# Kernel tuning notes

Hardware: AMD Instinct MI355X
Metric: run time of the kernel (lower is better)

## Reference

```python
import jax, jax.numpy as jnp
import numpy as np

D_MODEL, Q, V, H = 1024, 64, 64, 16
B, K = 2, 2048


def setup_inputs() -> dict:
    key = jax.random.key(0)
    ks = jax.random.split(key, 8)
    s = 0.02
    return {
        "xi": jax.random.normal(ks[0], (B, K, D_MODEL), dtype=jnp.float32),
        # stacked per-head projection weights (equivalent to h separate nn.Linear)
        "Wq": jax.random.normal(ks[1], (H, D_MODEL, Q), dtype=jnp.float32) * s,
        "bq": jax.random.normal(ks[2], (H, Q), dtype=jnp.float32) * s,
        "Wk": jax.random.normal(ks[3], (H, D_MODEL, Q), dtype=jnp.float32) * s,
        "bk": jax.random.normal(ks[4], (H, Q), dtype=jnp.float32) * s,
        "Wv": jax.random.normal(ks[5], (H, D_MODEL, V), dtype=jnp.float32) * s,
        "bv": jax.random.normal(ks[6], (H, V), dtype=jnp.float32) * s,
        "Wo": jax.random.normal(ks[7], (H * V, D_MODEL), dtype=jnp.float32) * s,
        "bo": jnp.zeros((D_MODEL,), dtype=jnp.float32),
    }


def reference(xi, Wq, bq, Wk, bk, Wv, bv, Wo, bo):
    # per-head projections, batched over heads: [B,H,K,q]
    queries = jnp.einsum("bkd,hdq->bhkq", xi, Wq) + bq[None, :, None, :]
    keys = jnp.einsum("bkd,hdq->bhkq", xi, Wk) + bk[None, :, None, :]
    values = jnp.einsum("bkd,hdv->bhkv", xi, Wv) + bv[None, :, None, :]
    # NOTE: original scales by sqrt(queries.shape[1]) == sqrt(seq_len K), not sqrt(q)
    scale = 1.0 / np.sqrt(xi.shape[1]).astype(np.float32)
    scores = jax.nn.softmax(jnp.einsum("bhkq,bhmq->bhkm", queries, keys) * scale, axis=-1)
    attn = jnp.einsum("bhkm,bhmv->bhkv", scores, values)  # [B,H,K,v]
    # concat heads along last dim -> [B,K,H*v]
    attn = attn.transpose(0, 2, 1, 3).reshape(xi.shape[0], xi.shape[1], -1)
    return attn @ Wo + bo
```

## Files before the change

kernel.cpp:

```cpp
#include <hip/hip_runtime.h>
#include <math.h>

typedef __bf16 bf16x8 __attribute__((ext_vector_type(8)));
typedef float  f32x4  __attribute__((ext_vector_type(4)));
typedef float  f32x16 __attribute__((ext_vector_type(16)));
typedef unsigned short u16x8 __attribute__((ext_vector_type(8)));

#define D_MODEL 1024
#define QDIM    64
#define HEADS   16
#define BATCH   2
#define SEQ     2048
#define M_ROWS  (BATCH*SEQ)
#define NCAT    (HEADS*3*QDIM)

__device__ __forceinline__ unsigned short f2bf(float f) {
    unsigned int u = __float_as_uint(f);
    u += 0x7fffu + ((u >> 16) & 1u);
    return (unsigned short)(u >> 16);
}

__device__ __forceinline__ void gl16(const unsigned short* g, unsigned short* l) {
    __builtin_amdgcn_global_load_lds(
        (const __attribute__((address_space(1))) unsigned int*)g,
        (__attribute__((address_space(3))) unsigned int*)l, 16, 0, 0);
}

__global__ __launch_bounds__(256) void k_cvt_bf16(const float* __restrict__ in,
                                                  unsigned short* __restrict__ out) {
    int i = (blockIdx.x * 256 + threadIdx.x) * 8;
    f32x4 a = *(const f32x4*)(in + i);
    f32x4 b = *(const f32x4*)(in + i + 4);
    u16x8 o;
    o[0]=f2bf(a[0]); o[1]=f2bf(a[1]); o[2]=f2bf(a[2]); o[3]=f2bf(a[3]);
    o[4]=f2bf(b[0]); o[5]=f2bf(b[1]); o[6]=f2bf(b[2]); o[7]=f2bf(b[3]);
    *(u16x8*)(out + i) = o;
}

__global__ __launch_bounds__(256) void k_prep_wcat(const float* __restrict__ Wq,
                                                   const float* __restrict__ Wk,
                                                   const float* __restrict__ Wv,
                                                   const float* __restrict__ bq,
                                                   const float* __restrict__ bk,
                                                   const float* __restrict__ bv,
                                                   unsigned short* __restrict__ WcatT,
                                                   float* __restrict__ bcat,
                                                   float qscale) {
    int blk = blockIdx.x;
    int dt = blk & 15, h = (blk >> 4) & 15, s = blk >> 8;
    const float* W = (s == 0) ? Wq : (s == 1) ? Wk : Wv;
    float sc = (s == 0) ? qscale : 1.0f;
    __shared__ float t[64][65];
    int tid = threadIdx.x;
    int dr = tid >> 2, qc = (tid & 3) * 16;
    const float* src = W + (size_t)h * (D_MODEL * QDIM) + (size_t)(dt * 64 + dr) * QDIM + qc;
#pragma unroll
    for (int j = 0; j < 4; ++j) {
        f32x4 v = *(const f32x4*)(src + j * 4);
        t[dr][qc + j * 4 + 0] = v[0]; t[dr][qc + j * 4 + 1] = v[1];
        t[dr][qc + j * 4 + 2] = v[2]; t[dr][qc + j * 4 + 3] = v[3];
    }
    __syncthreads();
    int q = tid >> 2, dc = (tid & 3) * 16;
    unsigned short* dst = WcatT + (size_t)(h * 192 + s * 64 + q) * D_MODEL + dt * 64 + dc;
#pragma unroll
    for (int j = 0; j < 2; ++j) {
        u16x8 o;
#pragma unroll
        for (int e = 0; e < 8; ++e) o[e] = f2bf(t[dc + j * 8 + e][q] * sc);
        *(u16x8*)(dst + j * 8) = o;
    }
    if (dt == 0 && tid < 64) {
        const float* bb = (s == 0) ? bq : (s == 1) ? bk : bv;
        bcat[h * 192 + s * 64 + tid] = bb[h * QDIM + tid] * sc;
    }
}

__global__ __launch_bounds__(256) void k_prep_wo(const float* __restrict__ Wo,
                                                 unsigned short* __restrict__ WoT) {
    int blk = blockIdx.x;
    int ct = blk & 15, rt = blk >> 4;
    __shared__ float t[64][65];
    int tid = threadIdx.x;
    int dr = tid >> 2, qc = (tid & 3) * 16;
    const float* src = Wo + (size_t)(rt * 64 + dr) * D_MODEL + ct * 64 + qc;
#pragma unroll
    for (int j = 0; j < 4; ++j) {
        f32x4 v = *(const f32x4*)(src + j * 4);
        t[dr][qc + j * 4 + 0] = v[0]; t[dr][qc + j * 4 + 1] = v[1];
        t[dr][qc + j * 4 + 2] = v[2]; t[dr][qc + j * 4 + 3] = v[3];
    }
    __syncthreads();
    int q = tid >> 2, dc = (tid & 3) * 16;
    unsigned short* dst = WoT + (size_t)(ct * 64 + q) * D_MODEL + rt * 64 + dc;
#pragma unroll
    for (int j = 0; j < 2; ++j) {
        u16x8 o;
#pragma unroll
        for (int e = 0; e < 8; ++e) o[e] = f2bf(t[dc + j * 8 + e][q]);
        *(u16x8*)(dst + j * 8) = o;
    }
}

template<bool OUT_BF16>
__global__ __launch_bounds__(256) void k_gemm(const unsigned short* __restrict__ A,
                                              const unsigned short* __restrict__ BT,
                                              const float* __restrict__ bias,
                                              void* __restrict__ Cout,
                                              int N, int Kd) {
    __shared__ __align__(16) unsigned short Alds[128 * 64];
    __shared__ __align__(16) unsigned short Blds[128 * 64];
    const int tid = threadIdx.x;
    const int lane = tid & 63, w = tid >> 6;
    const int g = lane >> 4, c = lane & 15;
    int nwg = gridDim.x * gridDim.y;
    int bid = blockIdx.y * gridDim.x + blockIdx.x;
    int sw = (bid & 7) * (nwg >> 3) + (bid >> 3);
    int bx = sw % gridDim.x, by = sw / gridDim.x;
    const int m0 = by * 128, n0 = bx * 128;
    const int wm = (w >> 1) * 64, wn = (w & 1) * 64;
    const int r8 = lane >> 3, chx = (lane & 7) ^ r8;
    const int swz = c & 7;
    f32x4 acc[4][4] = {};

    for (int k0 = 0; k0 < Kd; k0 += 64) {
        __builtin_amdgcn_sched_barrier(0);
        __builtin_amdgcn_s_barrier();
#pragma unroll
        for (int i = 0; i < 4; ++i) {
            int row = w * 32 + i * 8 + r8;
            gl16(A + (size_t)(m0 + row) * Kd + k0 + chx * 8, Alds + w * 2048 + i * 512);
            gl16(BT + (size_t)(n0 + row) * Kd + k0 + chx * 8, Blds + w * 2048 + i * 512);
        }
        asm volatile("s_waitcnt vmcnt(0)" ::: "memory");
        __builtin_amdgcn_s_barrier();
        __builtin_amdgcn_sched_barrier(0);
#pragma unroll
        for (int kk = 0; kk < 2; ++kk) {
            bf16x8 af[4], bfr[4];
#pragma unroll
            for (int mf = 0; mf < 4; ++mf) {
                int row = wm + mf * 16 + c;
                af[mf] = *(const bf16x8*)(Alds + row * 64 + (((kk * 4 + g) ^ swz) * 8));
            }
#pragma unroll
            for (int nf = 0; nf < 4; ++nf) {
                int row = wn + nf * 16 + c;
                bfr[nf] = *(const bf16x8*)(Blds + row * 64 + (((kk * 4 + g) ^ swz) * 8));
            }
            __builtin_amdgcn_s_setprio(1);
#pragma unroll
            for (int mf = 0; mf < 4; ++mf)
#pragma unroll
                for (int nf = 0; nf < 4; ++nf)
                    acc[mf][nf] = __builtin_amdgcn_mfma_f32_16x16x32_bf16(af[mf], bfr[nf], acc[mf][nf], 0, 0, 0);
            __builtin_amdgcn_s_setprio(0);
        }
    }

#pragma unroll
    for (int mf = 0; mf < 4; ++mf)
#pragma unroll
        for (int nf = 0; nf < 4; ++nf) {
            int col = n0 + wn + nf * 16 + c;
            float bb = bias[col];
#pragma unroll
            for (int r = 0; r < 4; ++r) {
                int row = m0 + wm + mf * 16 + 4 * g + r;
                float v = acc[mf][nf][r] + bb;
                if (OUT_BF16)
                    ((unsigned short*)Cout)[(size_t)row * N + col] = f2bf(v);
                else
                    ((float*)Cout)[(size_t)row * N + col] = v;
            }
        }
}

__global__ __launch_bounds__(256) void k_repack(const unsigned short* __restrict__ qkv,
                                                unsigned short* __restrict__ kfrag,
                                                unsigned short* __restrict__ vfrag) {
    int blk = blockIdx.x;
    int kt = blk & 31, h = (blk >> 5) & 15, b = blk >> 9;
    __shared__ unsigned short ktile[64][72];
    __shared__ unsigned short vtile[64][72];
    int tid = threadIdx.x;
#pragma unroll
    for (int j = 0; j < 2; ++j) {
        int cid = tid + j * 256;
        int row = cid >> 3, ch = (cid & 7) * 8;
        const unsigned short* base = qkv + (size_t)(b * SEQ + kt * 64 + row) * NCAT + h * 192;
        *(u16x8*)&ktile[row][ch] = *(const u16x8*)(base + 64 + ch);
        *(u16x8*)&vtile[row][ch] = *(const u16x8*)(base + 128 + ch);
    }
    __syncthreads();
    size_t obase = (size_t)blk * 4096;
#pragma unroll
    for (int j = 0; j < 2; ++j) {
        int p = tid + j * 256;
        int f = p >> 6, l31 = p & 31, hi = (p >> 5) & 1;
        *(u16x8*)(kfrag + obase + p * 8) =
            *(const u16x8*)&ktile[(f >> 2) * 32 + l31][(f & 3) * 16 + hi * 8];
        int vv = (f & 1) * 32 + l31;
        int k0 = (f >> 2) * 32 + ((f >> 1) & 1) * 16 + hi * 8;
        u16x8 o;
#pragma unroll
        for (int e = 0; e < 8; ++e) o[e] = vtile[k0 + e][vv];
        *(u16x8*)(vfrag + obase + p * 8) = o;
    }
}

__global__ __launch_bounds__(256) void k_attn(const unsigned short* __restrict__ qkv,
                                              const unsigned short* __restrict__ kfrag,
                                              const unsigned short* __restrict__ vfrag,
                                              unsigned short* __restrict__ attn) {
    int bid = blockIdx.x;
    int blk = (bid & 7) * 128 + (bid >> 3);
    int qt = blk & 31, h = (blk >> 5) & 15, b = blk >> 9;
    int tid = threadIdx.x, w = tid >> 6, lane = tid & 63;
    int l31 = lane & 31, hi = lane >> 5;
    int qh = w & 1, kh = w >> 1;

    __shared__ __align__(16) unsigned char KV[2][16384];

    const int qbase = b * SEQ + qt * 64;
    const unsigned short* qrow = qkv + (size_t)(qbase + qh * 32 + l31) * NCAT + h * 192;
    bf16x8 qf[4];
#pragma unroll
    for (int s = 0; s < 4; ++s) qf[s] = *(const bf16x8*)(qrow + s * 16 + hi * 8);

    f32x16 o0 = {}, o1 = {};
    float rsum = 0.f;

    const size_t fb = (size_t)(b * 512 + h * 32) * 4096;
    const unsigned short* ks0 = kfrag + fb + (w)     * 512 + lane * 8;
    const unsigned short* ks1 = kfrag + fb + (w + 4) * 512 + lane * 8;
    const unsigned short* vs0 = vfrag + fb + (w)     * 512 + lane * 8;
    const unsigned short* vs1 = vfrag + fb + (w + 4) * 512 + lane * 8;
    const unsigned kd0 = w * 1024, kd1 = (w + 4) * 1024;
    const unsigned vd0 = 8192 + w * 1024, vd1 = 8192 + (w + 4) * 1024;
    const int lx = lane * 16;

    gl16(ks0, (unsigned short*)&KV[0][kd0]);
    gl16(vs0, (unsigned short*)&KV[0][vd0]);
    gl16(ks1, (unsigned short*)&KV[0][kd1]);
    gl16(vs1, (unsigned short*)&KV[0][vd1]);
    ks0 += 4096; ks1 += 4096; vs0 += 4096; vs1 += 4096;
    asm volatile("s_waitcnt vmcnt(0)" ::: "memory");
    __builtin_amdgcn_s_barrier();

    const int NT = SEQ / 64;
    for (int t = 0; t < NT; ++t) {
        const int cur = t & 1;
        if (t + 1 < NT) {
            gl16(ks0, (unsigned short*)&KV[cur ^ 1][kd0]);
            gl16(vs0, (unsigned short*)&KV[cur ^ 1][vd0]);
            gl16(ks1, (unsigned short*)&KV[cur ^ 1][kd1]);
            gl16(vs1, (unsigned short*)&KV[cur ^ 1][vd1]);
            ks0 += 4096; ks1 += 4096; vs0 += 4096; vs1 += 4096;
            asm volatile("s_waitcnt vmcnt(4)" ::: "memory");
        } else {
            asm volatile("s_waitcnt vmcnt(0)" ::: "memory");
        }
        __builtin_amdgcn_s_barrier();
        __builtin_amdgcn_sched_barrier(0);

        const unsigned char* Kf = &KV[cur][0];
        const unsigned char* Vf = &KV[cur][8192];

        f32x16 st = {};
        __builtin_amdgcn_s_setprio(1);
#pragma unroll
        for (int s = 0; s < 4; ++s) {
            bf16x8 kf = *(const bf16x8*)(Kf + (kh * 4 + s) * 1024 + lx);
            st = __builtin_amdgcn_mfma_f32_32x32x16_bf16(kf, qf[s], st, 0, 0, 0);
        }
        __builtin_amdgcn_s_setprio(0);

#pragma unroll
        for (int r = 0; r < 16; ++r) {
            float p = __builtin_amdgcn_exp2f(st[r]);
            st[r] = p;
            rsum += p;
        }
        unsigned int d0, d1, d2, d3, d4, d5, d6, d7;
        asm("v_cvt_pk_bf16_f32 %0, %1, %2" : "=v"(d0) : "v"(st[0]),  "v"(st[1]));
        asm("v_cvt_pk_bf16_f32 %0, %1, %2" : "=v"(d1) : "v"(st[2]),  "v"(st[3]));
        asm("v_cvt_pk_bf16_f32 %0, %1, %2" : "=v"(d2) : "v"(st[4]),  "v"(st[5]));
        asm("v_cvt_pk_bf16_f32 %0, %1, %2" : "=v"(d3) : "v"(st[6]),  "v"(st[7]));
        asm("v_cvt_pk_bf16_f32 %0, %1, %2" : "=v"(d4) : "v"(st[8]),  "v"(st[9]));
        asm("v_cvt_pk_bf16_f32 %0, %1, %2" : "=v"(d5) : "v"(st[10]), "v"(st[11]));
        asm("v_cvt_pk_bf16_f32 %0, %1, %2" : "=v"(d6) : "v"(st[12]), "v"(st[13]));
        asm("v_cvt_pk_bf16_f32 %0, %1, %2" : "=v"(d7) : "v"(st[14]), "v"(st[15]));
        asm("v_permlane32_swap_b32 %0, %1" : "+v"(d0), "+v"(d2));
        asm("v_permlane32_swap_b32 %0, %1" : "+v"(d1), "+v"(d3));
        asm("v_permlane32_swap_b32 %0, %1" : "+v"(d4), "+v"(d6));
        asm("v_permlane32_swap_b32 %0, %1" : "+v"(d5), "+v"(d7));
        union { unsigned int u[4]; bf16x8 v; } pa0, pa1;
        pa0.u[0] = d0; pa0.u[1] = d1; pa0.u[2] = d2; pa0.u[3] = d3;
        pa1.u[0] = d4; pa1.u[1] = d5; pa1.u[2] = d6; pa1.u[3] = d7;

        __builtin_amdgcn_s_setprio(1);
        {
            bf16x8 vf00 = *(const bf16x8*)(Vf + (kh * 4 + 0) * 1024 + lx);
            bf16x8 vf01 = *(const bf16x8*)(Vf + (kh * 4 + 1) * 1024 + lx);
            bf16x8 vf10 = *(const bf16x8*)(Vf + (kh * 4 + 2) * 1024 + lx);
            bf16x8 vf11 = *(const bf16x8*)(Vf + (kh * 4 + 3) * 1024 + lx);
            o0 = __builtin_amdgcn_mfma_f32_32x32x16_bf16(pa0.v, vf00, o0, 0, 0, 0);
            o1 = __builtin_amdgcn_mfma_f32_32x32x16_bf16(pa0.v, vf01, o1, 0, 0, 0);
            o0 = __builtin_amdgcn_mfma_f32_32x32x16_bf16(pa1.v, vf10, o0, 0, 0, 0);
            o1 = __builtin_amdgcn_mfma_f32_32x32x16_bf16(pa1.v, vf11, o1, 0, 0, 0);
        }
        __builtin_amdgcn_s_setprio(0);
        __builtin_amdgcn_sched_barrier(0);
        __builtin_amdgcn_s_barrier();
    }

    rsum += __shfl_xor(rsum, 32);
    __syncthreads();
    float* red = (float*)&KV[0][0];
    float* rsb = (float*)&KV[1][0];
    if (kh == 1) {
#pragma unroll
        for (int r = 0; r < 16; ++r) {
            int q = (r & 3) + 8 * (r >> 2) + 4 * hi;
            red[(qh * 32 + q) * 64 + l31]      = o0[r];
            red[(qh * 32 + q) * 64 + 32 + l31] = o1[r];
        }
    }
    if (lane < 32) rsb[(kh * 2 + qh) * 32 + l31] = rsum;
    __syncthreads();
    if (kh == 0) {
#pragma unroll
        for (int r = 0; r < 16; ++r) {
            int q = (r & 3) + 8 * (r >> 2) + 4 * hi;
            float tot = rsb[qh * 32 + q] + rsb[(2 + qh) * 32 + q];
            float inv = 1.0f / tot;
            float v0 = (o0[r] + red[(qh * 32 + q) * 64 + l31]) * inv;
            float v1 = (o1[r] + red[(qh * 32 + q) * 64 + 32 + l31]) * inv;
            int row = qbase + qh * 32 + q;
            attn[(size_t)row * (HEADS * QDIM) + h * QDIM + l31]      = f2bf(v0);
            attn[(size_t)row * (HEADS * QDIM) + h * QDIM + 32 + l31] = f2bf(v1);
        }
    }
}

extern "C" void kernel_launch(void* const* d_in, const int* in_sizes, int n_in,
                              void* d_out, int out_size, void* d_ws, size_t ws_size,
                              hipStream_t stream) {
    const float* xi = (const float*)d_in[0];
    const float* Wq = (const float*)d_in[1];
    const float* bq = (const float*)d_in[2];
    const float* Wk = (const float*)d_in[3];
    const float* bk = (const float*)d_in[4];
    const float* Wv = (const float*)d_in[5];
    const float* bv = (const float*)d_in[6];
    const float* Wo = (const float*)d_in[7];
    const float* bo = (const float*)d_in[8];

    unsigned short* xi_bf = (unsigned short*)d_ws;
    unsigned short* WcatT = xi_bf + (size_t)M_ROWS * D_MODEL;
    unsigned short* WoT   = WcatT + (size_t)NCAT * D_MODEL;
    float*          bcat  = (float*)(WoT + (size_t)D_MODEL * D_MODEL);
    unsigned short* qkvc  = (unsigned short*)(bcat + NCAT);
    unsigned short* kfrag = qkvc + (size_t)M_ROWS * NCAT;
    unsigned short* vfrag = kfrag + (size_t)BATCH * HEADS * 32 * 4096;
    unsigned short* attnb = vfrag + (size_t)BATCH * HEADS * 32 * 4096;

    float qscale = 1.4426950408889634f / sqrtf((float)SEQ);

    k_cvt_bf16<<<(M_ROWS * D_MODEL) / 2048, 256, 0, stream>>>(xi, xi_bf);
    k_prep_wcat<<<768, 256, 0, stream>>>(Wq, Wk, Wv, bq, bk, bv, WcatT, bcat, qscale);
    k_prep_wo<<<256, 256, 0, stream>>>(Wo, WoT);

    k_gemm<true><<<dim3(NCAT / 128, M_ROWS / 128), 256, 0, stream>>>(
        xi_bf, WcatT, bcat, (void*)qkvc, NCAT, D_MODEL);

    k_repack<<<BATCH * HEADS * (SEQ / 64), 256, 0, stream>>>(qkvc, kfrag, vfrag);

    k_attn<<<BATCH * HEADS * (SEQ / 64), 256, 0, stream>>>(qkvc, kfrag, vfrag, attnb);

    k_gemm<false><<<dim3(D_MODEL / 128, M_ROWS / 128), 256, 0, stream>>>(
        attnb, WoT, bo, d_out, D_MODEL, D_MODEL);
}
```

Measured before the change: 129.5 us.

## Split attention key range in two with a separate reduction kernel

Each attention block now handles half of the key sequence, so twice as many blocks launch (2048 instead of 1024). Each block writes unnormalized fp32 partial outputs and row sums to a workspace. A new k_reduce kernel adds the two halves, normalizes and writes the bf16 attention output. This trades an extra launch and an fp32 partial-result round trip through memory for more parallelism across the GPU's compute units. It relies on the softmax needing no running max, which suggests the scores are bounded.

```diff
diff --git a/kernel.cpp b/kernel.cpp
--- a/kernel.cpp
+++ b/kernel.cpp
@@ -212,10 +212,12 @@
 __global__ __launch_bounds__(256) void k_attn(const unsigned short* __restrict__ qkv,
                                               const unsigned short* __restrict__ kfrag,
                                               const unsigned short* __restrict__ vfrag,
-                                              unsigned short* __restrict__ attn) {
+                                              float* __restrict__ po,
+                                              float* __restrict__ rs) {
     int bid = blockIdx.x;
-    int blk = (bid & 7) * 128 + (bid >> 3);
-    int qt = blk & 31, h = (blk >> 5) & 15, b = blk >> 9;
+    int blk = (bid & 7) * 256 + (bid >> 3);
+    int ks = blk & 1, rest = blk >> 1;
+    int qt = rest & 31, h = (rest >> 5) & 15, b = rest >> 9;
     int tid = threadIdx.x, w = tid >> 6, lane = tid & 63;
     int l31 = lane & 31, hi = lane >> 5;
     int qh = w & 1, kh = w >> 1;
@@ -231,7 +233,7 @@
     f32x16 o0 = {}, o1 = {};
     float rsum = 0.f;
 
-    const size_t fb = (size_t)(b * 512 + h * 32) * 4096;
+    const size_t fb = ((size_t)(b * 512 + h * 32) + ks * 16) * 4096;
     const unsigned short* ks0 = kfrag + fb + (w)     * 512 + lane * 8;
     const unsigned short* ks1 = kfrag + fb + (w + 4) * 512 + lane * 8;
     const unsigned short* vs0 = vfrag + fb + (w)     * 512 + lane * 8;
@@ -248,7 +250,7 @@
     asm volatile("s_waitcnt vmcnt(0)" ::: "memory");
     __builtin_amdgcn_s_barrier();
 
-    const int NT = SEQ / 64;
+    const int NT = 16;
     for (int t = 0; t < NT; ++t) {
         const int cur = t & 1;
         if (t + 1 < NT) {
@@ -329,18 +331,45 @@
     }
     if (lane < 32) rsb[(kh * 2 + qh) * 32 + l31] = rsum;
     __syncthreads();
+    float* pdst = po + (size_t)blk * 4096;
     if (kh == 0) {
 #pragma unroll
         for (int r = 0; r < 16; ++r) {
             int q = (r & 3) + 8 * (r >> 2) + 4 * hi;
-            float tot = rsb[qh * 32 + q] + rsb[(2 + qh) * 32 + q];
-            float inv = 1.0f / tot;
-            float v0 = (o0[r] + red[(qh * 32 + q) * 64 + l31]) * inv;
-            float v1 = (o1[r] + red[(qh * 32 + q) * 64 + 32 + l31]) * inv;
-            int row = qbase + qh * 32 + q;
-            attn[(size_t)row * (HEADS * QDIM) + h * QDIM + l31]      = f2bf(v0);
-            attn[(size_t)row * (HEADS * QDIM) + h * QDIM + 32 + l31] = f2bf(v1);
-        }
+            pdst[(qh * 32 + q) * 64 + l31]      = o0[r] + red[(qh * 32 + q) * 64 + l31];
+            pdst[(qh * 32 + q) * 64 + 32 + l31] = o1[r] + red[(qh * 32 + q) * 64 + 32 + l31];
+        }
+    }
+    if (tid < 64) {
+        int qq = tid & 31, qhh = tid >> 5;
+        rs[(size_t)blk * 64 + tid] = rsb[qhh * 32 + qq] + rsb[(2 + qhh) * 32 + qq];
+    }
+}
+
+__global__ __launch_bounds__(256) void k_reduce(const float* __restrict__ po,
+                                                const float* __restrict__ rs,
+                                                unsigned short* __restrict__ attn) {
+    int rest = blockIdx.x;
+    int qt = rest & 31, h = (rest >> 5) & 15, b = rest >> 9;
+    int tid = threadIdx.x;
+    int q = tid >> 2, vs = (tid & 3) * 16;
+    const float* p0 = po + ((size_t)rest * 2 + 0) * 4096 + q * 64 + vs;
+    const float* p1 = po + ((size_t)rest * 2 + 1) * 4096 + q * 64 + vs;
+    float inv = 1.0f / (rs[((size_t)rest * 2) * 64 + q] + rs[((size_t)rest * 2 + 1) * 64 + q]);
+    int row = b * SEQ + qt * 64 + q;
+    unsigned short* dst = attn + (size_t)row * (HEADS * QDIM) + h * 64 + vs;
+#pragma unroll
+    for (int j = 0; j < 2; ++j) {
+        f32x4 a0 = *(const f32x4*)(p0 + j * 8);
+        f32x4 a1 = *(const f32x4*)(p0 + j * 8 + 4);
+        f32x4 b0 = *(const f32x4*)(p1 + j * 8);
+        f32x4 b1 = *(const f32x4*)(p1 + j * 8 + 4);
+        u16x8 o;
+        o[0] = f2bf((a0[0] + b0[0]) * inv); o[1] = f2bf((a0[1] + b0[1]) * inv);
+        o[2] = f2bf((a0[2] + b0[2]) * inv); o[3] = f2bf((a0[3] + b0[3]) * inv);
+        o[4] = f2bf((a1[0] + b1[0]) * inv); o[5] = f2bf((a1[1] + b1[1]) * inv);
+        o[6] = f2bf((a1[2] + b1[2]) * inv); o[7] = f2bf((a1[3] + b1[3]) * inv);
+        *(u16x8*)(dst + j * 8) = o;
     }
 }
 
@@ -365,6 +394,8 @@
     unsigned short* kfrag = qkvc + (size_t)M_ROWS * NCAT;
     unsigned short* vfrag = kfrag + (size_t)BATCH * HEADS * 32 * 4096;
     unsigned short* attnb = vfrag + (size_t)BATCH * HEADS * 32 * 4096;
+    float*          po    = (float*)(attnb + (size_t)M_ROWS * (HEADS * QDIM));
+    float*          rsbuf = po + (size_t)2048 * 4096;
 
     float qscale = 1.4426950408889634f / sqrtf((float)SEQ);
 
@@ -377,7 +408,9 @@
 
     k_repack<<<BATCH * HEADS * (SEQ / 64), 256, 0, stream>>>(qkvc, kfrag, vfrag);
 
-    k_attn<<<BATCH * HEADS * (SEQ / 64), 256, 0, stream>>>(qkvc, kfrag, vfrag, attnb);
+    k_attn<<<2 * BATCH * HEADS * (SEQ / 64), 256, 0, stream>>>(qkvc, kfrag, vfrag, po, rsbuf);
+
+    k_reduce<<<BATCH * HEADS * (SEQ / 64), 256, 0, stream>>>(po, rsbuf, attnb);
 
     k_gemm<false><<<dim3(D_MODEL / 128, M_ROWS / 128), 256, 0, stream>>>(
         attnb, WoT, bo, d_out, D_MODEL, D_MODEL);
```

New measurement: 135.3 us. 4.5% more time.

## Pipeline GEMM K-loop with 4-stage LDS ring buffer and partial vmcnt waits

Applied to the files above, without the earlier changes.

Replaces the single-buffered 64-wide K-step GEMM loop with a 4-deep ring of 32-wide K tiles in a 64KB shared buffer. Loads for future stages are issued ahead and only partially waited on via vmcnt counts, so global-to-LDS transfers overlap with MFMA compute. The LDS swizzle and addressing are redone for the new tile shape. The larger LDS footprint may reduce occupancy per CU.

```diff
diff --git a/kernel.cpp b/kernel.cpp
--- a/kernel.cpp
+++ b/kernel.cpp
@@ -108,8 +108,7 @@
                                               const float* __restrict__ bias,
                                               void* __restrict__ Cout,
                                               int N, int Kd) {
-    __shared__ __align__(16) unsigned short Alds[128 * 64];
-    __shared__ __align__(16) unsigned short Blds[128 * 64];
+    __shared__ __align__(16) unsigned char smem[65536];
     const int tid = threadIdx.x;
     const int lane = tid & 63, w = tid >> 6;
     const int g = lane >> 4, c = lane & 15;
@@ -119,44 +118,75 @@
     int bx = sw % gridDim.x, by = sw / gridDim.x;
     const int m0 = by * 128, n0 = bx * 128;
     const int wm = (w >> 1) * 64, wn = (w & 1) * 64;
-    const int r8 = lane >> 3, chx = (lane & 7) ^ r8;
-    const int swz = c & 7;
     f32x4 acc[4][4] = {};
 
-    for (int k0 = 0; k0 < Kd; k0 += 64) {
+    const int srow = w * 16 + (lane >> 2);
+    const int scol = ((lane & 3) ^ ((lane >> 3) & 3)) * 8;
+    const unsigned short* pA0 = A  + (size_t)(m0 + srow) * Kd + scol;
+    const unsigned short* pA1 = pA0 + (size_t)64 * Kd;
+    const unsigned short* pB0 = BT + (size_t)(n0 + srow) * Kd + scol;
+    const unsigned short* pB1 = pB0 + (size_t)64 * Kd;
+    const int kc = (c >> 1) & 3;
+    const int aoff = (wm + c) * 64 + ((g ^ kc) * 16);
+    const int boff = (wn + c) * 64 + ((g ^ kc) * 16);
+
+#define STAGE(buf)                                                                   \
+    {                                                                                \
+        unsigned short* lb = (unsigned short*)(smem + (buf) * 16384) + w * 512;      \
+        gl16(pA0, lb);                                                               \
+        gl16(pA1, lb + 2048);                                                        \
+        gl16(pB0, lb + 4096);                                                        \
+        gl16(pB1, lb + 6144);                                                        \
+        pA0 += 32; pA1 += 32; pB0 += 32; pB1 += 32;                                  \
+    }
+
+#define COMPUTE(buf)                                                                 \
+    {                                                                                \
+        const unsigned char* Ab = smem + (buf) * 16384;                              \
+        const unsigned char* Bb = Ab + 8192;                                         \
+        bf16x8 af[4], bfr[4];                                                        \
+        _Pragma("unroll") for (int mf = 0; mf < 4; ++mf)                             \
+            af[mf] = *(const bf16x8*)(Ab + mf * 1024 + aoff);                        \
+        _Pragma("unroll") for (int nf = 0; nf < 4; ++nf)                             \
+            bfr[nf] = *(const bf16x8*)(Bb + nf * 1024 + boff);                       \
+        __builtin_amdgcn_s_setprio(1);                                               \
+        _Pragma("unroll") for (int mf = 0; mf < 4; ++mf)                             \
+            _Pragma("unroll") for (int nf = 0; nf < 4; ++nf)                         \
+                acc[mf][nf] = __builtin_amdgcn_mfma_f32_16x16x32_bf16(               \
+                    af[mf], bfr[nf], acc[mf][nf], 0, 0, 0);                          \
+        __builtin_amdgcn_s_setprio(0);                                               \
+    }
+
+    const int nt = Kd >> 5;
+    STAGE(0); STAGE(1); STAGE(2);
+
+    for (int t = 0; t < nt - 3; ++t) {
+        STAGE((t + 3) & 3);
+        asm volatile("s_waitcnt vmcnt(12)" ::: "memory");
+        __builtin_amdgcn_s_barrier();
+        __builtin_amdgcn_sched_barrier(0);
+        COMPUTE(t & 3);
         __builtin_amdgcn_sched_barrier(0);
         __builtin_amdgcn_s_barrier();
-#pragma unroll
-        for (int i = 0; i < 4; ++i) {
-            int row = w * 32 + i * 8 + r8;
-            gl16(A + (size_t)(m0 + row) * Kd + k0 + chx * 8, Alds + w * 2048 + i * 512);
-            gl16(BT + (size_t)(n0 + row) * Kd + k0 + chx * 8, Blds + w * 2048 + i * 512);
-        }
-        asm volatile("s_waitcnt vmcnt(0)" ::: "memory");
-        __builtin_amdgcn_s_barrier();
-        __builtin_amdgcn_sched_barrier(0);
-#pragma unroll
-        for (int kk = 0; kk < 2; ++kk) {
-            bf16x8 af[4], bfr[4];
-#pragma unroll
-            for (int mf = 0; mf < 4; ++mf) {
-                int row = wm + mf * 16 + c;
-                af[mf] = *(const bf16x8*)(Alds + row * 64 + (((kk * 4 + g) ^ swz) * 8));
-            }
-#pragma unroll
-            for (int nf = 0; nf < 4; ++nf) {
-                int row = wn + nf * 16 + c;
-                bfr[nf] = *(const bf16x8*)(Blds + row * 64 + (((kk * 4 + g) ^ swz) * 8));
-            }
-            __builtin_amdgcn_s_setprio(1);
-#pragma unroll
-            for (int mf = 0; mf < 4; ++mf)
-#pragma unroll
-                for (int nf = 0; nf < 4; ++nf)
-                    acc[mf][nf] = __builtin_amdgcn_mfma_f32_16x16x32_bf16(af[mf], bfr[nf], acc[mf][nf], 0, 0, 0);
-            __builtin_amdgcn_s_setprio(0);
-        }
-    }
+    }
+    asm volatile("s_waitcnt vmcnt(8)" ::: "memory");
+    __builtin_amdgcn_s_barrier();
+    __builtin_amdgcn_sched_barrier(0);
+    COMPUTE((nt - 3) & 3);
+    __builtin_amdgcn_sched_barrier(0);
+    __builtin_amdgcn_s_barrier();
+    asm volatile("s_waitcnt vmcnt(4)" ::: "memory");
+    __builtin_amdgcn_s_barrier();
+    __builtin_amdgcn_sched_barrier(0);
+    COMPUTE((nt - 2) & 3);
+    __builtin_amdgcn_sched_barrier(0);
+    __builtin_amdgcn_s_barrier();
+    asm volatile("s_waitcnt vmcnt(0)" ::: "memory");
+    __builtin_amdgcn_s_barrier();
+    __builtin_amdgcn_sched_barrier(0);
+    COMPUTE((nt - 1) & 3);
+#undef STAGE
+#undef COMPUTE
 
 #pragma unroll
     for (int mf = 0; mf < 4; ++mf)
```

Measured after the change: 127.1 us. No clear change (-1.9%).
